# Kernel optimization log

Measured on AMD Instinct MI355X. Metric: run time of the kernel, lower is better.

## Reference

```python
import jax, jax.numpy as jnp
import numpy as np

B, N, E, Q = 4, 10000, 160000, 256
D, M, U, H, P = 128, 64, 126, 128, 7  # node_dim, msg_sz, update_sz, mlp hidden, pose dim
MSG_STEPS = 3
NUM_COPIES = 1


def setup_inputs() -> dict:
    key = jax.random.key(0)
    ks = jax.random.split(key, 12)
    return {
        "nodes_states": jax.random.normal(ks[0], (B, N, D), jnp.float32),
        "query_poses": jax.random.normal(ks[1], (B, Q, P), jnp.float32),
        "attn": jax.random.uniform(ks[2], (B, Q, N), jnp.float32) / N,
        "edge_sources": jax.random.randint(ks[3], (E,), 0, N),
        "edge_sinks": jax.random.randint(ks[4], (E,), 0, N),
        "w1e": jax.random.normal(ks[5], (2 * D, H), jnp.float32) * 0.05,
        "b1e": jnp.zeros((H,), jnp.float32),
        "w2e": jax.random.normal(ks[6], (H, M), jnp.float32) * 0.05,
        "b2e": jnp.zeros((M,), jnp.float32),
        "w1n": jax.random.normal(ks[7], (D + M, H), jnp.float32) * 0.05,
        "b1n": jnp.zeros((H,), jnp.float32),
        "w2n": jax.random.normal(ks[8], (H, U), jnp.float32) * 0.05,
        "b2n": jnp.zeros((U,), jnp.float32),
    }


def reference(nodes_states, query_poses, attn, edge_sources, edge_sinks,
              w1e, b1e, w2e, b2e, w1n, b1n, w2n, b2n):
    def step(states, _):
        # gather endpoint states: [B, E, 2*D]
        einp = jnp.concatenate([states[:, edge_sources], states[:, edge_sinks]], axis=-1)
        # edge MLP -> per-edge messages [B, E, M]
        msg = jax.nn.relu(einp @ w1e + b1e) @ w2e + b2e
        # scatter-add messages to sink nodes [B, N, M]
        incoming = jnp.zeros((states.shape[0], N, M), states.dtype).at[:, edge_sinks].add(msg)
        # node MLP update [B, N, U]
        ninp = jnp.concatenate([incoming, states], axis=-1)
        upd = jax.nn.relu(ninp @ w1n + b1n) @ w2n + b2n
        # only the last U channels (state part, not positions) are updated
        states = states.at[:, :, -U:].add(upd)
        return states, None

    states, _ = jax.lax.scan(step, nodes_states, None, length=MSG_STEPS)
    extraction = jnp.einsum('bqn,bnd->bqd', attn, states)  # interpolation readout
    return jnp.concatenate([query_poses] * NUM_COPIES + [extraction], axis=-1)
```

## Files before the change

kernel.cpp:

```cpp
#include <hip/hip_runtime.h>

#define Bx 4
#define Nn 10000
#define Ee 160000
#define Qq 256
#define Dd 128
#define Mm 64
#define Uu 126
#define Hh 128
#define Pp 7

#define KG 1252

typedef unsigned short u16;
typedef __bf16 bf16x8 __attribute__((ext_vector_type(8)));
typedef float f32x4 __attribute__((ext_vector_type(4)));

__device__ __forceinline__ float b2f(u16 h){
  unsigned u = ((unsigned)h) << 16; float f; __builtin_memcpy(&f, &u, 4); return f;
}
__device__ __forceinline__ u16 f2b(float f){
  __bf16 h = (__bf16)f; u16 r; __builtin_memcpy(&r, &h, 2); return r;
}
__device__ __forceinline__ float ldin(const void* p, long i, int flag){
  return flag ? b2f(((const u16*)p)[i]) : ((const float*)p)[i];
}

__global__ void probe_kernel(const void* in0, int* flag){
  if (threadIdx.x == 0 && blockIdx.x == 0){
    const u16* p = (const u16*)in0;
    int cnt = 0;
    for (int i = 0; i < 256; i++){
      float a = fabsf(b2f(p[i]));
      if (a > 0.0009765625f && a < 32.0f) cnt++;
    }
    *flag = (cnt >= 240) ? 1 : 0;
  }
}

__global__ void prep_kernel(const void* w1e, const void* b1e, const void* w2e, const void* b2e,
                            const void* w1n, const void* b1n, const void* w2n, const void* b2n,
                            const int* __restrict__ flag,
                            u16* w1e_s, u16* w2e_s, u16* w1n_s, u16* w2n_s,
                            float* b1e_f, float* b2e_f, float* b1n_f, float* b2n_f)
{
  int f = *flag;
  for (int idx = blockIdx.x * blockDim.x + threadIdx.x; idx < 82368; idx += gridDim.x * blockDim.x){
    if (idx < 32768){
      int k = idx >> 7, h = idx & 127;
      w1e_s[(k >> 3) * 1024 + h * 8 + (k & 7)] = f2b(ldin(w1e, idx, f));
    } else if (idx < 40960){
      int i2 = idx - 32768; int k = i2 >> 6, m2 = i2 & 63;
      w2e_s[(k >> 3) * 512 + m2 * 8 + (k & 7)] = f2b(ldin(w2e, i2, f));
    } else if (idx < 65536){
      int i2 = idx - 40960; int k = i2 >> 7, h = i2 & 127;
      w1n_s[(k >> 3) * 1024 + h * 8 + (k & 7)] = f2b(ldin(w1n, i2, f));
    } else if (idx < 81920){
      int i2 = idx - 65536; int k = i2 >> 7, u = i2 & 127;
      float v = (u < 126) ? ldin(w2n, (long)k * 126 + u, f) : 0.f;
      w2n_s[(k >> 3) * 1024 + u * 8 + (k & 7)] = f2b(v);
    } else if (idx < 82048){ b1e_f[idx - 81920] = ldin(b1e, idx - 81920, f); }
    else if (idx < 82112){ b2e_f[idx - 82048] = ldin(b2e, idx - 82048, f); }
    else if (idx < 82240){ b1n_f[idx - 82112] = ldin(b1n, idx - 82112, f); }
    else { int j = idx - 82240; b2n_f[j] = (j < 126) ? ldin(b2n, j, f) : 0.f; }
  }
}

__global__ void init_states_kernel(const void* in0, const int* __restrict__ flag,
                                   const int* __restrict__ snk,
                                   float* __restrict__ sf, u16* __restrict__ sbm,
                                   int* __restrict__ cnt)
{
  int f = *flag;
  const long total = (long)Bx * Nn * Dd;
  long base = (long)blockIdx.x * blockDim.x + threadIdx.x;
  for (long i = base; i < total; i += (long)gridDim.x * blockDim.x){
    float v = ldin(in0, i, f);
    sf[i] = v; sbm[i] = f2b(v);
  }
  for (long i = base; i < Ee; i += (long)gridDim.x * blockDim.x)
    atomicAdd(&cnt[snk[(int)i]], 1);
}

__global__ void scan_kernel(const int* __restrict__ cnt, int* __restrict__ rowp){
  __shared__ int tot[1024];
  int t = threadIdx.x;
  int base = t * 10;
  int local[10]; int s = 0;
  #pragma unroll
  for (int i = 0; i < 10; i++){
    int v = (base + i < Nn) ? cnt[base + i] : 0;
    local[i] = s; s += v;
  }
  tot[t] = s;
  __syncthreads();
  for (int o = 1; o < 1024; o <<= 1){
    int v = (t >= o) ? tot[t - o] : 0;
    __syncthreads();
    tot[t] += v;
    __syncthreads();
  }
  int prefix = (t == 0) ? 0 : tot[t - 1];
  #pragma unroll
  for (int i = 0; i < 10; i++)
    if (base + i < Nn) rowp[base + i] = prefix + local[i];
  if (t == 1023) rowp[Nn] = tot[1023];
}
__global__ void fill_kernel(const int* __restrict__ src, const int* __restrict__ snk,
                            const int* __restrict__ rowp, int* __restrict__ cnt,
                            int* __restrict__ psrc){
  int i = blockIdx.x * blockDim.x + threadIdx.x;
  if (i < Ee){
    int s = snk[i];
    int p = rowp[s] + atomicAdd(&cnt[s], 1);
    psrc[p] = src[i];
  }
}

__global__ __launch_bounds__(256) void xform_kernel(
  const u16* __restrict__ sbm, const u16* __restrict__ w1s,
  const float* __restrict__ b1f, u16* __restrict__ xab)
{
  __shared__ __align__(16) u16 w1h[16384];
  __shared__ __align__(16) u16 Yt[64 * 136];
  int tid = threadIdx.x;
  int b = (blockIdx.x & 7) >> 1;
  int nt = ((blockIdx.x >> 3) << 1) + (blockIdx.x & 1);
  if (nt >= 157) return;
  int n0 = nt * 64;
  int w = tid >> 6, lane = tid & 63, m = lane & 15, quad = lane >> 4;
  int n = n0 + w * 16 + m;
  int nld = n < Nn ? n : Nn - 1;
  const u16* srow = sbm + (((size_t)b * Nn + nld) << 7);

  bf16x8 a[4];
  #pragma unroll
  for (int lk = 0; lk < 4; lk++) a[lk] = *(const bf16x8*)(srow + lk * 32 + quad * 8);

  const f32x4 z4 = {0.f, 0.f, 0.f, 0.f};
  int row_l = lane >> 2, seg = lane & 3;
  int nst = n0 + w * 16 + row_l;

  #pragma unroll
  for (int half = 0; half < 2; half++){
    __syncthreads();
    {
      const uint4* g = (const uint4*)(w1s + half * 16384);
      uint4* l = (uint4*)w1h;
      #pragma unroll
      for (int i = 0; i < 8; i++) l[tid + i * 256] = g[tid + i * 256];
    }
    __syncthreads();
    f32x4 acc[8];
    #pragma unroll
    for (int ct = 0; ct < 8; ct++) acc[ct] = z4;
    #pragma unroll
    for (int lk = 0; lk < 4; lk++){
      #pragma unroll
      for (int ct = 0; ct < 8; ct++){
        bf16x8 bv = *(const bf16x8*)(w1h + (((lk * 4 + quad) << 7) + ct * 16 + m) * 8);
        acc[ct] = __builtin_amdgcn_mfma_f32_16x16x32_bf16(a[lk], bv, acc[ct], 0, 0, 0);
      }
    }
    #pragma unroll
    for (int ct = 0; ct < 8; ct++){
      float bb = (half == 0) ? b1f[ct * 16 + m] : 0.f;
      #pragma unroll
      for (int i = 0; i < 4; i++)
        Yt[(w * 16 + quad * 4 + i) * 136 + ct * 16 + m] = f2b(acc[ct][i] + bb);
    }
    if (nst < Nn){
      const uint4* tp = (const uint4*)(Yt + (w * 16 + row_l) * 136 + seg * 32);
      uint4 x0 = tp[0], x1 = tp[1], x2 = tp[2], x3 = tp[3];
      uint4* gp = (uint4*)(xab + ((size_t)b * Nn + nst) * 256 + half * 128 + seg * 32);
      gp[0] = x0; gp[1] = x1; gp[2] = x2; gp[3] = x3;
    }
  }
}

__global__ __launch_bounds__(256) void node_kernel(
  float* __restrict__ sf, u16* __restrict__ sbm, const u16* __restrict__ xab,
  const int* __restrict__ rowp, const int* __restrict__ psrc,
  const u16* __restrict__ w2es, const float* __restrict__ b2ef,
  const u16* __restrict__ w1s, const u16* __restrict__ w2s,
  const float* __restrict__ b1f, const float* __restrict__ b2f2)
{
  __shared__ __align__(16) u16 ninp[64 * 200];
  __shared__ __align__(16) u16 hsYt[64 * 136];
  int b = (blockIdx.x & 7) >> 1;
  int nt = ((blockIdx.x >> 3) << 1) + (blockIdx.x & 1);
  if (nt >= 157) return;
  int n0 = nt * 64;
  int tid = threadIdx.x;

  {
    int nl = tid >> 2, part = tid & 3;
    int n = n0 + nl;
    float acc[32];
    #pragma unroll
    for (int i = 0; i < 32; i++) acc[i] = 0.f;
    if (n < Nn){
      float xbf[32];
      {
        const uint4* xp = (const uint4*)(xab + ((size_t)b * Nn + n) * 256 + 128 + part * 32);
        union { uint4 v; u16 h[8]; } q[4];
        q[0].v = xp[0]; q[1].v = xp[1]; q[2].v = xp[2]; q[3].v = xp[3];
        #pragma unroll
        for (int t4 = 0; t4 < 4; t4++)
          #pragma unroll
          for (int j = 0; j < 8; j++) xbf[t4 * 8 + j] = b2f(q[t4].h[j]);
      }
      int r0 = rowp[n], r1 = rowp[n + 1];
      const u16* xb0 = xab + (size_t)b * Nn * 256;
      for (int r = r0; r < r1; r++){
        int s = psrc[r];
        const uint4* xp = (const uint4*)(xb0 + (size_t)s * 256 + part * 32);
        union { uint4 v; u16 h[8]; } q[4];
        q[0].v = xp[0]; q[1].v = xp[1]; q[2].v = xp[2]; q[3].v = xp[3];
        #pragma unroll
        for (int t4 = 0; t4 < 4; t4++)
          #pragma unroll
          for (int j = 0; j < 8; j++){
            float v = b2f(q[t4].h[j]) + xbf[t4 * 8 + j];
            acc[t4 * 8 + j] += v > 0.f ? v : 0.f;
          }
      }
    }
    union { u16 h[32]; uint4 v[4]; } hb;
    #pragma unroll
    for (int i = 0; i < 32; i++) hb.h[i] = f2b(acc[i]);
    uint4* hp = (uint4*)(hsYt + nl * 136 + part * 32);
    hp[0] = hb.v[0]; hp[1] = hb.v[1]; hp[2] = hb.v[2]; hp[3] = hb.v[3];
    uint4* dp = (uint4*)(ninp + nl * 200 + 64 + part * 32);
    if (n < Nn){
      const uint4* sp = (const uint4*)(sbm + (((size_t)b * Nn + n) << 7) + part * 32);
      #pragma unroll
      for (int i = 0; i < 4; i++) dp[i] = sp[i];
    } else {
      uint4 zz = {0, 0, 0, 0};
      #pragma unroll
      for (int i = 0; i < 4; i++) dp[i] = zz;
    }
  }

  int w = tid >> 6, lane = tid & 63, m = lane & 15, quad = lane >> 4;
  const f32x4 z4 = {0.f, 0.f, 0.f, 0.f};

  {
    f32x4 acc[4];
    #pragma unroll
    for (int ct = 0; ct < 4; ct++) acc[ct] = z4;
    #pragma unroll
    for (int ks = 0; ks < 4; ks++){
      bf16x8 a = *(const bf16x8*)(hsYt + (w * 16 + m) * 136 + ks * 32 + quad * 8);
      #pragma unroll
      for (int ct = 0; ct < 4; ct++){
        bf16x8 bv = *(const bf16x8*)(w2es + (((ks * 4 + quad) << 6) + ct * 16 + m) * 8);
        acc[ct] = __builtin_amdgcn_mfma_f32_16x16x32_bf16(a, bv, acc[ct], 0, 0, 0);
      }
    }
    #pragma unroll
    for (int i = 0; i < 4; i++){
      int n = n0 + w * 16 + quad * 4 + i;
      float deg = (n < Nn) ? (float)(rowp[n + 1] - rowp[n]) : 0.f;
      #pragma unroll
      for (int ct = 0; ct < 4; ct++)
        ninp[(w * 16 + quad * 4 + i) * 200 + ct * 16 + m] = f2b(acc[ct][i] + deg * b2ef[ct * 16 + m]);
    }
  }

  f32x4 acc1[8];
  #pragma unroll
  for (int ct = 0; ct < 8; ct++) acc1[ct] = z4;
  #pragma unroll 1
  for (int ks = 0; ks < 6; ks++){
    bf16x8 a = *(const bf16x8*)(ninp + (w * 16 + m) * 200 + ks * 32 + quad * 8);
    #pragma unroll
    for (int ct = 0; ct < 8; ct++){
      bf16x8 bv = *(const bf16x8*)(w1s + (((ks * 4 + quad) << 7) + ct * 16 + m) * 8);
      acc1[ct] = __builtin_amdgcn_mfma_f32_16x16x32_bf16(a, bv, acc1[ct], 0, 0, 0);
    }
  }
  #pragma unroll
  for (int ct = 0; ct < 8; ct++){
    float bb = b1f[ct * 16 + m];
    #pragma unroll
    for (int i = 0; i < 4; i++){
      float v = acc1[ct][i] + bb;
      v = v > 0.f ? v : 0.f;
      hsYt[(w * 16 + quad * 4 + i) * 136 + ct * 16 + m] = f2b(v);
    }
  }
  f32x4 acc2[8];
  #pragma unroll
  for (int ct = 0; ct < 8; ct++) acc2[ct] = z4;
  #pragma unroll 1
  for (int ko = 0; ko < 4; ko++){
    bf16x8 a2 = *(const bf16x8*)(hsYt + (w * 16 + m) * 136 + ko * 32 + quad * 8);
    #pragma unroll
    for (int ct = 0; ct < 8; ct++){
      bf16x8 bv = *(const bf16x8*)(w2s + (((ko * 4 + quad) << 7) + ct * 16 + m) * 8);
      acc2[ct] = __builtin_amdgcn_mfma_f32_16x16x32_bf16(a2, bv, acc2[ct], 0, 0, 0);
    }
  }
  #pragma unroll
  for (int ct = 0; ct < 8; ct++){
    int u = ct * 16 + m;
    if (u < 126){
      float bb = b2f2[u];
      #pragma unroll
      for (int i = 0; i < 4; i++){
        int n = n0 + w * 16 + quad * 4 + i;
        if (n < Nn){
          size_t idx = (((size_t)b * Nn + n) << 7) + 2 + u;
          float v = sf[idx] + acc2[ct][i] + bb;
          sf[idx] = v;
          sbm[idx] = f2b(v);
        }
      }
    }
  }
}

__global__ void swz_s_kernel(const u16* __restrict__ sbm, u16* __restrict__ sswz)
{
  const long total = (long)Bx * KG * 128;
  for (long i = (long)blockIdx.x * blockDim.x + threadIdx.x; i < total; i += (long)gridDim.x * blockDim.x){
    int d = (int)(i & 127); long r = i >> 7;
    int kg = (int)(r % KG); int b = (int)(r / KG);
    union { u16 h[8]; uint4 v[2]; } t;
    if (kg < 1250){
      #pragma unroll
      for (int j = 0; j < 8; j++)
        t.h[j] = sbm[(((size_t)b * Nn + kg * 8 + j) << 7) + d];
    } else {
      #pragma unroll
      for (int j = 0; j < 8; j++) t.h[j] = 0;
    }
    *(uint4*)(sswz + i * 8) = t.v[0];
    *(uint4*)(sswz + i * 8 + 8) = t.v[1];
  }
}
__global__ __launch_bounds__(256) void extract2_kernel(
  const void* __restrict__ attn, const int* __restrict__ flag,
  const u16* __restrict__ sswz, float* __restrict__ part)
{
  int f = *flag;
  int blk = blockIdx.x;
  int kc = blk & 31, qt = (blk >> 5) & 3, b = blk >> 7;
  int tid = threadIdx.x, w = tid >> 6, lane = tid & 63, m = lane & 15, quad = lane >> 4;
  int qr = qt * 4 + w, q0 = qr * 16;
  int kg0 = kc * 40;
  int nsteps = (kc == 31) ? 3 : 10;
  long arow = ((long)(b * Qq + q0 + m)) * Nn;
  const u16* ab16 = (const u16*)attn + arow;
  const float* af32 = (const float*)attn + arow;
  const u16* sbase = sswz + ((size_t)b) * KG * 1024;
  f32x4 acc[8];
  const f32x4 z4 = {0.f, 0.f, 0.f, 0.f};
  #pragma unroll
  for (int ct = 0; ct < 8; ct++) acc[ct] = z4;
  #pragma unroll 1
  for (int t = 0; t < nsteps; t++){
    int kg = kg0 + t * 4 + quad;
    int kgc = kg < KG ? kg : 0;
    bf16x8 a;
    if (kg < 1250){
      if (f){
        a = *(const bf16x8*)(ab16 + kg * 8);
      } else {
        const float* ap = af32 + kg * 8;
        float4 p0 = *(const float4*)ap;
        float4 p1 = *(const float4*)(ap + 4);
        a[0] = (__bf16)p0.x; a[1] = (__bf16)p0.y; a[2] = (__bf16)p0.z; a[3] = (__bf16)p0.w;
        a[4] = (__bf16)p1.x; a[5] = (__bf16)p1.y; a[6] = (__bf16)p1.z; a[7] = (__bf16)p1.w;
      }
    } else {
      #pragma unroll
      for (int j = 0; j < 8; j++) a[j] = (__bf16)0.f;
    }
    #pragma unroll
    for (int ct = 0; ct < 8; ct++){
      bf16x8 bv = *(const bf16x8*)(sbase + ((size_t)kgc * 128 + ct * 16 + m) * 8);
      acc[ct] = __builtin_amdgcn_mfma_f32_16x16x32_bf16(a, bv, acc[ct], 0, 0, 0);
    }
  }
  #pragma unroll
  for (int ct = 0; ct < 8; ct++){
    #pragma unroll
    for (int i = 0; i < 4; i++)
      part[(((size_t)(kc * 4 + b)) * Qq + q0 + quad * 4 + i) * 128 + ct * 16 + m] = acc[ct][i];
  }
}

__global__ void final_kernel(const void* __restrict__ poses, const int* __restrict__ flag,
                             const float* __restrict__ part, void* __restrict__ out)
{
  int f = *flag;
  const long total = (long)Bx * Qq * (Pp + Dd);
  for (long idx = (long)blockIdx.x * blockDim.x + threadIdx.x; idx < total; idx += (long)gridDim.x * blockDim.x){
    int j = (int)(idx % (Pp + Dd));
    long bq = idx / (Pp + Dd);
    float v;
    if (j < Pp){
      v = ldin(poses, bq * Pp + j, f);
    } else {
      int dd = j - Pp;
      int b = (int)(bq >> 8), q = (int)(bq & 255);
      v = 0.f;
      #pragma unroll
      for (int kc = 0; kc < 32; kc++)
        v += part[(((size_t)(kc * 4 + b) * Qq + q) << 7) + dd];
    }
    if (f) ((u16*)out)[idx] = f2b(v);
    else ((float*)out)[idx] = v;
  }
}

extern "C" void kernel_launch(void* const* d_in, const int* in_sizes, int n_in,
                              void* d_out, int out_size, void* d_ws, size_t ws_size,
                              hipStream_t stream)
{
  const void* in_states = d_in[0];
  const void* in_poses  = d_in[1];
  const void* in_attn   = d_in[2];
  const int*  in_src    = (const int*)d_in[3];
  const int*  in_snk    = (const int*)d_in[4];
  const void* in_w1e = d_in[5];  const void* in_b1e = d_in[6];
  const void* in_w2e = d_in[7];  const void* in_b2e = d_in[8];
  const void* in_w1n = d_in[9];  const void* in_b1n = d_in[10];
  const void* in_w2n = d_in[11]; const void* in_b2n = d_in[12];

  char* ws = (char*)d_ws;
  size_t off = 0;
  auto alloc = [&](size_t bytes){ size_t o = off; off = (off + bytes + 255) & ~(size_t)255; return o; };
  size_t o_sf   = alloc((size_t)Bx * Nn * Dd * 4);
  size_t o_sb   = alloc((size_t)Bx * Nn * Dd * 2);
  size_t o_xab  = alloc((size_t)Bx * Nn * 256 * 2);
  size_t o_rowp = alloc((size_t)(Nn + 1) * 4);
  size_t o_rcnt = alloc((size_t)Nn * 4);
  size_t o_psrc = alloc((size_t)Ee * 4);
  size_t o_w1e  = alloc(32768 * 2);
  size_t o_w2e  = alloc(8192 * 2);
  size_t o_w1n  = alloc(24576 * 2);
  size_t o_w2n  = alloc(16384 * 2);
  size_t o_b1e  = alloc(128 * 4);
  size_t o_b2e  = alloc(64 * 4);
  size_t o_b1n  = alloc(128 * 4);
  size_t o_b2n  = alloc(128 * 4);
  size_t o_flag = alloc(4);

  size_t sswzB = (size_t)Bx * KG * 128 * 8 * 2;
  size_t partB = (size_t)32 * Bx * Qq * Dd * 4;
  size_t o_sswz = alloc(sswzB);
  size_t o_part = alloc(partB);

  float* sf    = (float*)(ws + o_sf);
  u16*   sbm   = (u16*)(ws + o_sb);
  u16*   xab   = (u16*)(ws + o_xab);
  int*   rowp  = (int*)(ws + o_rowp);
  int*   rcnt  = (int*)(ws + o_rcnt);
  int*   psrc  = (int*)(ws + o_psrc);
  u16*   w1e_s = (u16*)(ws + o_w1e);
  u16*   w2e_s = (u16*)(ws + o_w2e);
  u16*   w1n_s = (u16*)(ws + o_w1n);
  u16*   w2n_s = (u16*)(ws + o_w2n);
  float* b1e_f = (float*)(ws + o_b1e);
  float* b2e_f = (float*)(ws + o_b2e);
  float* b1n_f = (float*)(ws + o_b1n);
  float* b2n_f = (float*)(ws + o_b2n);
  int*   flag  = (int*)(ws + o_flag);
  u16*   sswz  = (u16*)(ws + o_sswz);
  float* part  = (float*)(ws + o_part);

  hipMemsetAsync(rcnt, 0, (size_t)Nn * 4, stream);
  probe_kernel<<<1, 64, 0, stream>>>(in_states, flag);
  prep_kernel<<<322, 256, 0, stream>>>(in_w1e, in_b1e, in_w2e, in_b2e,
                                       in_w1n, in_b1n, in_w2n, in_b2n, flag,
                                       w1e_s, w2e_s, w1n_s, w2n_s,
                                       b1e_f, b2e_f, b1n_f, b2n_f);
  init_states_kernel<<<1024, 256, 0, stream>>>(in_states, flag, in_snk, sf, sbm, rcnt);

  scan_kernel<<<1, 1024, 0, stream>>>(rcnt, rowp);
  hipMemsetAsync(rcnt, 0, (size_t)Nn * 4, stream);
  fill_kernel<<<(Ee + 255) / 256, 256, 0, stream>>>(in_src, in_snk, rowp, rcnt, psrc);

  for (int step = 0; step < 3; step++){
    xform_kernel<<<632, 256, 0, stream>>>(sbm, w1e_s, b1e_f, xab);
    node_kernel<<<632, 256, 0, stream>>>(sf, sbm, xab, rowp, psrc,
                                         w2e_s, b2e_f,
                                         w1n_s, w2n_s, b1n_f, b2n_f);
  }
  swz_s_kernel<<<2504, 256, 0, stream>>>(sbm, sswz);
  extract2_kernel<<<512, 256, 0, stream>>>(in_attn, flag, sswz, part);
  final_kernel<<<540, 256, 0, stream>>>(in_poses, flag, part, d_out);
}
```

Before: 375.8 us.

## Split edge-transform buffer, halve node tile, and unroll neighbor gather by four

The interleaved xab buffer becomes two separate arrays, xa (source half) and xb (sink half), so the per-edge gather reads a compact 256-byte row stride. The node kernel now handles 32 nodes per block with 8 threads per node, launches twice as many blocks, and unrolls the CSR neighbor loop four-wide with masked duplicate loads so more gathers are in flight. The xb-half writes and the final sf/sbm updates use nontemporal stores and loads. In exchange, half of each block's threads sit idle during the MFMA phase, and a 4-edge unroll wastes loads on short neighbor lists.

Result: slower. 445.4 us (+18.5%).

```diff
diff --git a/kernel.cpp b/kernel.cpp
--- a/kernel.cpp
+++ b/kernel.cpp
@@ -15,6 +15,7 @@
 typedef unsigned short u16;
 typedef __bf16 bf16x8 __attribute__((ext_vector_type(8)));
 typedef float f32x4 __attribute__((ext_vector_type(4)));
+typedef unsigned int u32x4 __attribute__((ext_vector_type(4)));
 
 __device__ __forceinline__ float b2f(u16 h){
   unsigned u = ((unsigned)h) << 16; float f; __builtin_memcpy(&f, &u, 4); return f;
@@ -119,7 +120,7 @@
 
 __global__ __launch_bounds__(256) void xform_kernel(
   const u16* __restrict__ sbm, const u16* __restrict__ w1s,
-  const float* __restrict__ b1f, u16* __restrict__ xab)
+  const float* __restrict__ b1f, u16* __restrict__ xa, u16* __restrict__ xb)
 {
   __shared__ __align__(16) u16 w1h[16384];
   __shared__ __align__(16) u16 Yt[64 * 136];
@@ -170,78 +171,118 @@
         Yt[(w * 16 + quad * 4 + i) * 136 + ct * 16 + m] = f2b(acc[ct][i] + bb);
     }
     if (nst < Nn){
-      const uint4* tp = (const uint4*)(Yt + (w * 16 + row_l) * 136 + seg * 32);
-      uint4 x0 = tp[0], x1 = tp[1], x2 = tp[2], x3 = tp[3];
-      uint4* gp = (uint4*)(xab + ((size_t)b * Nn + nst) * 256 + half * 128 + seg * 32);
-      gp[0] = x0; gp[1] = x1; gp[2] = x2; gp[3] = x3;
+      const u16* tb = Yt + (w * 16 + row_l) * 136 + seg * 8;
+      u32x4 x0 = *(const u32x4*)(tb);
+      u32x4 x1 = *(const u32x4*)(tb + 32);
+      u32x4 x2 = *(const u32x4*)(tb + 64);
+      u32x4 x3 = *(const u32x4*)(tb + 96);
+      u16* gb = (half == 0 ? xa : xb) + ((size_t)b * Nn + nst) * 128 + seg * 8;
+      if (half == 0){
+        *(u32x4*)(gb)      = x0;
+        *(u32x4*)(gb + 32) = x1;
+        *(u32x4*)(gb + 64) = x2;
+        *(u32x4*)(gb + 96) = x3;
+      } else {
+        __builtin_nontemporal_store(x0, (u32x4*)(gb));
+        __builtin_nontemporal_store(x1, (u32x4*)(gb + 32));
+        __builtin_nontemporal_store(x2, (u32x4*)(gb + 64));
+        __builtin_nontemporal_store(x3, (u32x4*)(gb + 96));
+      }
     }
   }
 }
 
 __global__ __launch_bounds__(256) void node_kernel(
-  float* __restrict__ sf, u16* __restrict__ sbm, const u16* __restrict__ xab,
+  float* __restrict__ sf, u16* __restrict__ sbm,
+  const u16* __restrict__ xa, const u16* __restrict__ xb,
   const int* __restrict__ rowp, const int* __restrict__ psrc,
   const u16* __restrict__ w2es, const float* __restrict__ b2ef,
   const u16* __restrict__ w1s, const u16* __restrict__ w2s,
   const float* __restrict__ b1f, const float* __restrict__ b2f2)
 {
-  __shared__ __align__(16) u16 ninp[64 * 200];
-  __shared__ __align__(16) u16 hsYt[64 * 136];
+  __shared__ __align__(16) u16 ninp[32 * 200];
+  __shared__ __align__(16) u16 hsYt[32 * 136];
   int b = (blockIdx.x & 7) >> 1;
   int nt = ((blockIdx.x >> 3) << 1) + (blockIdx.x & 1);
-  if (nt >= 157) return;
-  int n0 = nt * 64;
+  int n0 = nt * 32;
+  if (n0 >= Nn + 31) return;
   int tid = threadIdx.x;
 
   {
-    int nl = tid >> 2, part = tid & 3;
+    int nl = tid >> 3, part = tid & 7;
     int n = n0 + nl;
-    float acc[32];
-    #pragma unroll
-    for (int i = 0; i < 32; i++) acc[i] = 0.f;
+    float acc[16];
+    #pragma unroll
+    for (int i = 0; i < 16; i++) acc[i] = 0.f;
     if (n < Nn){
-      float xbf[32];
+      float xbf[16];
       {
-        const uint4* xp = (const uint4*)(xab + ((size_t)b * Nn + n) * 256 + 128 + part * 32);
-        union { uint4 v; u16 h[8]; } q[4];
-        q[0].v = xp[0]; q[1].v = xp[1]; q[2].v = xp[2]; q[3].v = xp[3];
+        const u16* xp = xb + ((size_t)b * Nn + n) * 128 + part * 8;
+        union { uint4 v; u16 h[8]; } q0, q1;
+        q0.v = *(const uint4*)(xp);
+        q1.v = *(const uint4*)(xp + 64);
         #pragma unroll
-        for (int t4 = 0; t4 < 4; t4++)
-          #pragma unroll
-          for (int j = 0; j < 8; j++) xbf[t4 * 8 + j] = b2f(q[t4].h[j]);
-      }
-      int r0 = rowp[n], r1 = rowp[n + 1];
-      const u16* xb0 = xab + (size_t)b * Nn * 256;
-      for (int r = r0; r < r1; r++){
-        int s = psrc[r];
-        const uint4* xp = (const uint4*)(xb0 + (size_t)s * 256 + part * 32);
-        union { uint4 v; u16 h[8]; } q[4];
-        q[0].v = xp[0]; q[1].v = xp[1]; q[2].v = xp[2]; q[3].v = xp[3];
+        for (int j = 0; j < 8; j++){ xbf[j] = b2f(q0.h[j]); xbf[8 + j] = b2f(q1.h[j]); }
+      }
+      int r0v = rowp[n], r1v = rowp[n + 1];
+      const u16* xaB = xa + (size_t)b * Nn * 128 + part * 8;
+      for (int r = r0v; r < r1v; r += 4){
+        int rb = r + 1 < r1v ? r + 1 : r0v;
+        int rc = r + 2 < r1v ? r + 2 : r0v;
+        int rd = r + 3 < r1v ? r + 3 : r0v;
+        float wb = r + 1 < r1v ? 1.f : 0.f;
+        float wc = r + 2 < r1v ? 1.f : 0.f;
+        float wd = r + 3 < r1v ? 1.f : 0.f;
+        int sa = psrc[r], sb2 = psrc[rb], sc = psrc[rc], sd = psrc[rd];
+        const u16* pa = xaB + (size_t)sa * 128;
+        const u16* pb = xaB + (size_t)sb2 * 128;
+        const u16* pc = xaB + (size_t)sc * 128;
+        const u16* pd = xaB + (size_t)sd * 128;
+        union { uint4 v; u16 h[8]; } qa0, qa1, qb0, qb1, qc0, qc1, qd0, qd1;
+        qa0.v = *(const uint4*)(pa); qa1.v = *(const uint4*)(pa + 64);
+        qb0.v = *(const uint4*)(pb); qb1.v = *(const uint4*)(pb + 64);
+        qc0.v = *(const uint4*)(pc); qc1.v = *(const uint4*)(pc + 64);
+        qd0.v = *(const uint4*)(pd); qd1.v = *(const uint4*)(pd + 64);
         #pragma unroll
-        for (int t4 = 0; t4 < 4; t4++)
-          #pragma unroll
-          for (int j = 0; j < 8; j++){
-            float v = b2f(q[t4].h[j]) + xbf[t4 * 8 + j];
-            acc[t4 * 8 + j] += v > 0.f ? v : 0.f;
-          }
-      }
-    }
-    union { u16 h[32]; uint4 v[4]; } hb;
-    #pragma unroll
-    for (int i = 0; i < 32; i++) hb.h[i] = f2b(acc[i]);
-    uint4* hp = (uint4*)(hsYt + nl * 136 + part * 32);
-    hp[0] = hb.v[0]; hp[1] = hb.v[1]; hp[2] = hb.v[2]; hp[3] = hb.v[3];
-    uint4* dp = (uint4*)(ninp + nl * 200 + 64 + part * 32);
+        for (int j = 0; j < 8; j++){
+          float va0 = b2f(qa0.h[j]) + xbf[j];
+          float va1 = b2f(qa1.h[j]) + xbf[8 + j];
+          acc[j]     += va0 > 0.f ? va0 : 0.f;
+          acc[8 + j] += va1 > 0.f ? va1 : 0.f;
+          float vb0 = b2f(qb0.h[j]) + xbf[j];
+          float vb1 = b2f(qb1.h[j]) + xbf[8 + j];
+          acc[j]     = fmaf(wb, vb0 > 0.f ? vb0 : 0.f, acc[j]);
+          acc[8 + j] = fmaf(wb, vb1 > 0.f ? vb1 : 0.f, acc[8 + j]);
+          float vc0 = b2f(qc0.h[j]) + xbf[j];
+          float vc1 = b2f(qc1.h[j]) + xbf[8 + j];
+          acc[j]     = fmaf(wc, vc0 > 0.f ? vc0 : 0.f, acc[j]);
+          acc[8 + j] = fmaf(wc, vc1 > 0.f ? vc1 : 0.f, acc[8 + j]);
+          float vd0 = b2f(qd0.h[j]) + xbf[j];
+          float vd1 = b2f(qd1.h[j]) + xbf[8 + j];
+          acc[j]     = fmaf(wd, vd0 > 0.f ? vd0 : 0.f, acc[j]);
+          acc[8 + j] = fmaf(wd, vd1 > 0.f ? vd1 : 0.f, acc[8 + j]);
+        }
+      }
+    }
+    union { u16 h[16]; uint4 v[2]; } hb;
+    #pragma unroll
+    for (int i = 0; i < 16; i++) hb.h[i] = f2b(acc[i]);
+    u16* hp = hsYt + nl * 136 + part * 8;
+    *(uint4*)(hp)      = hb.v[0];
+    *(uint4*)(hp + 64) = hb.v[1];
+    u16* dp = ninp + nl * 200 + 64 + part * 8;
     if (n < Nn){
-      const uint4* sp = (const uint4*)(sbm + (((size_t)b * Nn + n) << 7) + part * 32);
-      #pragma unroll
-      for (int i = 0; i < 4; i++) dp[i] = sp[i];
+      const u16* sp = sbm + (((size_t)b * Nn + n) << 7) + part * 8;
+      *(uint4*)(dp)      = *(const uint4*)(sp);
+      *(uint4*)(dp + 64) = *(const uint4*)(sp + 64);
     } else {
       uint4 zz = {0, 0, 0, 0};
-      #pragma unroll
-      for (int i = 0; i < 4; i++) dp[i] = zz;
-    }
-  }
+      *(uint4*)(dp)      = zz;
+      *(uint4*)(dp + 64) = zz;
+    }
+  }
+  __syncthreads();
+  if (tid >= 128) return;
 
   int w = tid >> 6, lane = tid & 63, m = lane & 15, quad = lane >> 4;
   const f32x4 z4 = {0.f, 0.f, 0.f, 0.f};
@@ -313,9 +354,9 @@
         int n = n0 + w * 16 + quad * 4 + i;
         if (n < Nn){
           size_t idx = (((size_t)b * Nn + n) << 7) + 2 + u;
-          float v = sf[idx] + acc2[ct][i] + bb;
-          sf[idx] = v;
-          sbm[idx] = f2b(v);
+          float v = __builtin_nontemporal_load(&sf[idx]) + acc2[ct][i] + bb;
+          __builtin_nontemporal_store(v, &sf[idx]);
+          __builtin_nontemporal_store(f2b(v), &sbm[idx]);
         }
       }
     }
@@ -436,7 +477,8 @@
   auto alloc = [&](size_t bytes){ size_t o = off; off = (off + bytes + 255) & ~(size_t)255; return o; };
   size_t o_sf   = alloc((size_t)Bx * Nn * Dd * 4);
   size_t o_sb   = alloc((size_t)Bx * Nn * Dd * 2);
-  size_t o_xab  = alloc((size_t)Bx * Nn * 256 * 2);
+  size_t o_xa   = alloc((size_t)Bx * Nn * 128 * 2);
+  size_t o_xb   = alloc((size_t)Bx * Nn * 128 * 2);
   size_t o_rowp = alloc((size_t)(Nn + 1) * 4);
   size_t o_rcnt = alloc((size_t)Nn * 4);
   size_t o_psrc = alloc((size_t)Ee * 4);
@@ -457,7 +499,8 @@
 
   float* sf    = (float*)(ws + o_sf);
   u16*   sbm   = (u16*)(ws + o_sb);
-  u16*   xab   = (u16*)(ws + o_xab);
+  u16*   xa    = (u16*)(ws + o_xa);
+  u16*   xb    = (u16*)(ws + o_xb);
   int*   rowp  = (int*)(ws + o_rowp);
   int*   rcnt  = (int*)(ws + o_rcnt);
   int*   psrc  = (int*)(ws + o_psrc);
@@ -486,10 +529,10 @@
   fill_kernel<<<(Ee + 255) / 256, 256, 0, stream>>>(in_src, in_snk, rowp, rcnt, psrc);
 
   for (int step = 0; step < 3; step++){
-    xform_kernel<<<632, 256, 0, stream>>>(sbm, w1e_s, b1e_f, xab);
-    node_kernel<<<632, 256, 0, stream>>>(sf, sbm, xab, rowp, psrc,
-                                         w2e_s, b2e_f,
-                                         w1n_s, w2n_s, b1n_f, b2n_f);
+    xform_kernel<<<632, 256, 0, stream>>>(sbm, w1e_s, b1e_f, xa, xb);
+    node_kernel<<<1256, 256, 0, stream>>>(sf, sbm, xa, xb, rowp, psrc,
+                                          w2e_s, b2e_f,
+                                          w1n_s, w2n_s, b1n_f, b2n_f);
   }
   swz_s_kernel<<<2504, 256, 0, stream>>>(sbm, sswz);
   extract2_kernel<<<512, 256, 0, stream>>>(in_attn, flag, sswz, part);
```

## Store gathered edge pre-activations in FP8 and halve node tile size

Applied to the files above, without the earlier changes.

The per-source half of the first edge-MLP layer (gathered once per edge) is now written as FP8 with a permuted column order, and the w2e swizzle is changed to match. The sink half stays bf16 in a separate buffer. The intent is to halve the bytes of the irregular per-edge gather, which dominates node_kernel. The node kernel also processes 32 nodes per block with 8 threads per node, over twice as many blocks, and only half its threads run the MLP stage. The tradeoff is lower precision on the edge pre-activations, plus idle threads in the MFMA phase.

New measurement: 370.3 us. Within noise of the previous version (-1.5%).

```diff
diff --git a/kernel.cpp b/kernel.cpp
--- a/kernel.cpp
+++ b/kernel.cpp
@@ -15,6 +15,7 @@
 typedef unsigned short u16;
 typedef __bf16 bf16x8 __attribute__((ext_vector_type(8)));
 typedef float f32x4 __attribute__((ext_vector_type(4)));
+typedef float f32x2 __attribute__((ext_vector_type(2)));
 
 __device__ __forceinline__ float b2f(u16 h){
   unsigned u = ((unsigned)h) << 16; float f; __builtin_memcpy(&f, &u, 4); return f;
@@ -51,7 +52,7 @@
       w1e_s[(k >> 3) * 1024 + h * 8 + (k & 7)] = f2b(ldin(w1e, idx, f));
     } else if (idx < 40960){
       int i2 = idx - 32768; int k = i2 >> 6, m2 = i2 & 63;
-      w2e_s[(k >> 3) * 512 + m2 * 8 + (k & 7)] = f2b(ldin(w2e, i2, f));
+      w2e_s[(k & 15) * 512 + m2 * 8 + (k >> 4)] = f2b(ldin(w2e, i2, f));
     } else if (idx < 65536){
       int i2 = idx - 40960; int k = i2 >> 7, h = i2 & 127;
       w1n_s[(k >> 3) * 1024 + h * 8 + (k & 7)] = f2b(ldin(w1n, i2, f));
@@ -119,10 +120,9 @@
 
 __global__ __launch_bounds__(256) void xform_kernel(
   const u16* __restrict__ sbm, const u16* __restrict__ w1s,
-  const float* __restrict__ b1f, u16* __restrict__ xab)
+  const float* __restrict__ b1f, unsigned char* __restrict__ xa, u16* __restrict__ xb)
 {
   __shared__ __align__(16) u16 w1h[16384];
-  __shared__ __align__(16) u16 Yt[64 * 136];
   int tid = threadIdx.x;
   int b = (blockIdx.x & 7) >> 1;
   int nt = ((blockIdx.x >> 3) << 1) + (blockIdx.x & 1);
@@ -138,8 +138,10 @@
   for (int lk = 0; lk < 4; lk++) a[lk] = *(const bf16x8*)(srow + lk * 32 + quad * 8);
 
   const f32x4 z4 = {0.f, 0.f, 0.f, 0.f};
-  int row_l = lane >> 2, seg = lane & 3;
-  int nst = n0 + w * 16 + row_l;
+  int rbase = n0 + w * 16 + quad * 4;
+  float bb[8];
+  #pragma unroll
+  for (int ct = 0; ct < 8; ct++) bb[ct] = b1f[ct * 16 + m];
 
   #pragma unroll
   for (int half = 0; half < 2; half++){
@@ -162,86 +164,104 @@
         acc[ct] = __builtin_amdgcn_mfma_f32_16x16x32_bf16(a[lk], bv, acc[ct], 0, 0, 0);
       }
     }
-    #pragma unroll
-    for (int ct = 0; ct < 8; ct++){
-      float bb = (half == 0) ? b1f[ct * 16 + m] : 0.f;
-      #pragma unroll
-      for (int i = 0; i < 4; i++)
-        Yt[(w * 16 + quad * 4 + i) * 136 + ct * 16 + m] = f2b(acc[ct][i] + bb);
-    }
-    if (nst < Nn){
-      const uint4* tp = (const uint4*)(Yt + (w * 16 + row_l) * 136 + seg * 32);
-      uint4 x0 = tp[0], x1 = tp[1], x2 = tp[2], x3 = tp[3];
-      uint4* gp = (uint4*)(xab + ((size_t)b * Nn + nst) * 256 + half * 128 + seg * 32);
-      gp[0] = x0; gp[1] = x1; gp[2] = x2; gp[3] = x3;
+    if (half == 0){
+      #pragma unroll
+      for (int i = 0; i < 4; i++){
+        int r = rbase + i;
+        if (r < Nn){
+          int d0 = __builtin_amdgcn_cvt_pk_fp8_f32(acc[0][i] + bb[0], acc[1][i] + bb[1], 0, false);
+          d0 = __builtin_amdgcn_cvt_pk_fp8_f32(acc[2][i] + bb[2], acc[3][i] + bb[3], d0, true);
+          int d1 = __builtin_amdgcn_cvt_pk_fp8_f32(acc[4][i] + bb[4], acc[5][i] + bb[5], 0, false);
+          d1 = __builtin_amdgcn_cvt_pk_fp8_f32(acc[6][i] + bb[6], acc[7][i] + bb[7], d1, true);
+          uint2 v; v.x = (unsigned)d0; v.y = (unsigned)d1;
+          *(uint2*)(xa + ((size_t)b * Nn + r) * 128 + m * 8) = v;
+        }
+      }
+    } else {
+      #pragma unroll
+      for (int i = 0; i < 4; i++){
+        int r = rbase + i;
+        if (r < Nn){
+          union { u16 h[8]; uint4 v; } t;
+          #pragma unroll
+          for (int ct = 0; ct < 8; ct++) t.h[ct] = f2b(acc[ct][i]);
+          *(uint4*)(xb + ((size_t)b * Nn + r) * 128 + m * 8) = t.v;
+        }
+      }
     }
   }
 }
 
 __global__ __launch_bounds__(256) void node_kernel(
-  float* __restrict__ sf, u16* __restrict__ sbm, const u16* __restrict__ xab,
+  float* __restrict__ sf, u16* __restrict__ sbm,
+  const unsigned char* __restrict__ xa, const u16* __restrict__ xb,
   const int* __restrict__ rowp, const int* __restrict__ psrc,
   const u16* __restrict__ w2es, const float* __restrict__ b2ef,
   const u16* __restrict__ w1s, const u16* __restrict__ w2s,
   const float* __restrict__ b1f, const float* __restrict__ b2f2)
 {
-  __shared__ __align__(16) u16 ninp[64 * 200];
-  __shared__ __align__(16) u16 hsYt[64 * 136];
+  __shared__ __align__(16) u16 ninp[32 * 200];
+  __shared__ __align__(16) u16 hsYt[32 * 136];
   int b = (blockIdx.x & 7) >> 1;
   int nt = ((blockIdx.x >> 3) << 1) + (blockIdx.x & 1);
-  if (nt >= 157) return;
-  int n0 = nt * 64;
+  int n0 = nt * 32;
+  if (n0 >= Nn + 31) return;
   int tid = threadIdx.x;
 
   {
-    int nl = tid >> 2, part = tid & 3;
+    int nl = tid >> 3, part = tid & 7;
     int n = n0 + nl;
-    float acc[32];
-    #pragma unroll
-    for (int i = 0; i < 32; i++) acc[i] = 0.f;
+    float acc[16];
+    #pragma unroll
+    for (int i = 0; i < 16; i++) acc[i] = 0.f;
     if (n < Nn){
-      float xbf[32];
+      float xbf[16];
       {
-        const uint4* xp = (const uint4*)(xab + ((size_t)b * Nn + n) * 256 + 128 + part * 32);
-        union { uint4 v; u16 h[8]; } q[4];
-        q[0].v = xp[0]; q[1].v = xp[1]; q[2].v = xp[2]; q[3].v = xp[3];
+        const u16* xp = xb + ((size_t)b * Nn + n) * 128 + part * 16;
+        union { uint4 v; u16 h[8]; } q0, q1;
+        q0.v = *(const uint4*)(xp);
+        q1.v = *(const uint4*)(xp + 8);
         #pragma unroll
-        for (int t4 = 0; t4 < 4; t4++)
-          #pragma unroll
-          for (int j = 0; j < 8; j++) xbf[t4 * 8 + j] = b2f(q[t4].h[j]);
-      }
-      int r0 = rowp[n], r1 = rowp[n + 1];
-      const u16* xb0 = xab + (size_t)b * Nn * 256;
-      for (int r = r0; r < r1; r++){
+        for (int j = 0; j < 8; j++){ xbf[j] = b2f(q0.h[j]); xbf[8 + j] = b2f(q1.h[j]); }
+      }
+      int r0v = rowp[n], r1v = rowp[n + 1];
+      const unsigned char* xaB = xa + (size_t)b * Nn * 128 + part * 16;
+      for (int r = r0v; r < r1v; r++){
         int s = psrc[r];
-        const uint4* xp = (const uint4*)(xb0 + (size_t)s * 256 + part * 32);
-        union { uint4 v; u16 h[8]; } q[4];
-        q[0].v = xp[0]; q[1].v = xp[1]; q[2].v = xp[2]; q[3].v = xp[3];
-        #pragma unroll
-        for (int t4 = 0; t4 < 4; t4++)
-          #pragma unroll
-          for (int j = 0; j < 8; j++){
-            float v = b2f(q[t4].h[j]) + xbf[t4 * 8 + j];
-            acc[t4 * 8 + j] += v > 0.f ? v : 0.f;
-          }
-      }
-    }
-    union { u16 h[32]; uint4 v[4]; } hb;
-    #pragma unroll
-    for (int i = 0; i < 32; i++) hb.h[i] = f2b(acc[i]);
-    uint4* hp = (uint4*)(hsYt + nl * 136 + part * 32);
-    hp[0] = hb.v[0]; hp[1] = hb.v[1]; hp[2] = hb.v[2]; hp[3] = hb.v[3];
-    uint4* dp = (uint4*)(ninp + nl * 200 + 64 + part * 32);
+        uint4 q = *(const uint4*)(xaB + (size_t)s * 128);
+        #define ACC4(W, B) { \
+          f32x2 lo = __builtin_amdgcn_cvt_pk_f32_fp8((int)(W), false); \
+          f32x2 hi = __builtin_amdgcn_cvt_pk_f32_fp8((int)(W), true);  \
+          float v0 = lo[0] + xbf[B + 0]; acc[B + 0] += fmaxf(v0, 0.f); \
+          float v1 = lo[1] + xbf[B + 1]; acc[B + 1] += fmaxf(v1, 0.f); \
+          float v2 = hi[0] + xbf[B + 2]; acc[B + 2] += fmaxf(v2, 0.f); \
+          float v3 = hi[1] + xbf[B + 3]; acc[B + 3] += fmaxf(v3, 0.f); }
+        ACC4(q.x, 0)
+        ACC4(q.y, 4)
+        ACC4(q.z, 8)
+        ACC4(q.w, 12)
+        #undef ACC4
+      }
+    }
+    union { u16 h[16]; uint4 v[2]; } hb;
+    #pragma unroll
+    for (int i = 0; i < 16; i++) hb.h[i] = f2b(acc[i]);
+    u16* hp = hsYt + nl * 136 + part * 16;
+    *(uint4*)(hp)     = hb.v[0];
+    *(uint4*)(hp + 8) = hb.v[1];
+    u16* dp = ninp + nl * 200 + 64 + part * 16;
     if (n < Nn){
-      const uint4* sp = (const uint4*)(sbm + (((size_t)b * Nn + n) << 7) + part * 32);
-      #pragma unroll
-      for (int i = 0; i < 4; i++) dp[i] = sp[i];
+      const u16* sp = sbm + (((size_t)b * Nn + n) << 7) + part * 16;
+      *(uint4*)(dp)     = *(const uint4*)(sp);
+      *(uint4*)(dp + 8) = *(const uint4*)(sp + 8);
     } else {
       uint4 zz = {0, 0, 0, 0};
-      #pragma unroll
-      for (int i = 0; i < 4; i++) dp[i] = zz;
-    }
-  }
+      *(uint4*)(dp)     = zz;
+      *(uint4*)(dp + 8) = zz;
+    }
+  }
+  __syncthreads();
+  if (tid >= 128) return;
 
   int w = tid >> 6, lane = tid & 63, m = lane & 15, quad = lane >> 4;
   const f32x4 z4 = {0.f, 0.f, 0.f, 0.f};
@@ -436,7 +456,8 @@
   auto alloc = [&](size_t bytes){ size_t o = off; off = (off + bytes + 255) & ~(size_t)255; return o; };
   size_t o_sf   = alloc((size_t)Bx * Nn * Dd * 4);
   size_t o_sb   = alloc((size_t)Bx * Nn * Dd * 2);
-  size_t o_xab  = alloc((size_t)Bx * Nn * 256 * 2);
+  size_t o_xa   = alloc((size_t)Bx * Nn * 128);
+  size_t o_xb   = alloc((size_t)Bx * Nn * 128 * 2);
   size_t o_rowp = alloc((size_t)(Nn + 1) * 4);
   size_t o_rcnt = alloc((size_t)Nn * 4);
   size_t o_psrc = alloc((size_t)Ee * 4);
@@ -457,7 +478,8 @@
 
   float* sf    = (float*)(ws + o_sf);
   u16*   sbm   = (u16*)(ws + o_sb);
-  u16*   xab   = (u16*)(ws + o_xab);
+  unsigned char* xa = (unsigned char*)(ws + o_xa);
+  u16*   xb    = (u16*)(ws + o_xb);
   int*   rowp  = (int*)(ws + o_rowp);
   int*   rcnt  = (int*)(ws + o_rcnt);
   int*   psrc  = (int*)(ws + o_psrc);
@@ -486,10 +508,10 @@
   fill_kernel<<<(Ee + 255) / 256, 256, 0, stream>>>(in_src, in_snk, rowp, rcnt, psrc);
 
   for (int step = 0; step < 3; step++){
-    xform_kernel<<<632, 256, 0, stream>>>(sbm, w1e_s, b1e_f, xab);
-    node_kernel<<<632, 256, 0, stream>>>(sf, sbm, xab, rowp, psrc,
-                                         w2e_s, b2e_f,
-                                         w1n_s, w2n_s, b1n_f, b2n_f);
+    xform_kernel<<<632, 256, 0, stream>>>(sbm, w1e_s, b1e_f, xa, xb);
+    node_kernel<<<1256, 256, 0, stream>>>(sf, sbm, xa, xb, rowp, psrc,
+                                          w2e_s, b2e_f,
+                                          w1n_s, w2n_s, b1n_f, b2n_f);
   }
   swz_s_kernel<<<2504, 256, 0, stream>>>(sbm, sswz);
   extract2_kernel<<<512, 256, 0, stream>>>(in_attn, flag, sswz, part);
```

## Process all batches per node tile so edge gather reuses CSR traversal

Applied to the files above, without the earlier changes.

Splits the transformed edge-input buffer into separate source and sink planes, and reorganises node_kernel so each block handles 16 nodes across all 4 batches instead of 64 nodes of one batch. Each CSR edge list (rowp/psrc) is traversed once and gathers all four batch rows per source, with 16 lanes per node covering the 128 channels. This amortises index loads and improves gather coalescing. The cost is more register pressure from four accumulator sets and a different block-to-row mapping in the MFMA stages, where the wave index now selects the batch.

New measurement: 379.3 us. No clear change (+0.9%).

```diff
diff --git a/kernel.cpp b/kernel.cpp
--- a/kernel.cpp
+++ b/kernel.cpp
@@ -119,7 +119,7 @@
 
 __global__ __launch_bounds__(256) void xform_kernel(
   const u16* __restrict__ sbm, const u16* __restrict__ w1s,
-  const float* __restrict__ b1f, u16* __restrict__ xab)
+  const float* __restrict__ b1f, u16* __restrict__ xa, u16* __restrict__ xb)
 {
   __shared__ __align__(16) u16 w1h[16384];
   __shared__ __align__(16) u16 Yt[64 * 136];
@@ -170,16 +170,23 @@
         Yt[(w * 16 + quad * 4 + i) * 136 + ct * 16 + m] = f2b(acc[ct][i] + bb);
     }
     if (nst < Nn){
-      const uint4* tp = (const uint4*)(Yt + (w * 16 + row_l) * 136 + seg * 32);
-      uint4 x0 = tp[0], x1 = tp[1], x2 = tp[2], x3 = tp[3];
-      uint4* gp = (uint4*)(xab + ((size_t)b * Nn + nst) * 256 + half * 128 + seg * 32);
-      gp[0] = x0; gp[1] = x1; gp[2] = x2; gp[3] = x3;
+      const u16* tb = Yt + (w * 16 + row_l) * 136 + seg * 8;
+      uint4 x0 = *(const uint4*)(tb);
+      uint4 x1 = *(const uint4*)(tb + 32);
+      uint4 x2 = *(const uint4*)(tb + 64);
+      uint4 x3 = *(const uint4*)(tb + 96);
+      u16* gb = (half == 0 ? xa : xb) + ((size_t)b * Nn + nst) * 128 + seg * 8;
+      *(uint4*)(gb)      = x0;
+      *(uint4*)(gb + 32) = x1;
+      *(uint4*)(gb + 64) = x2;
+      *(uint4*)(gb + 96) = x3;
     }
   }
 }
 
 __global__ __launch_bounds__(256) void node_kernel(
-  float* __restrict__ sf, u16* __restrict__ sbm, const u16* __restrict__ xab,
+  float* __restrict__ sf, u16* __restrict__ sbm,
+  const u16* __restrict__ xa, const u16* __restrict__ xb,
   const int* __restrict__ rowp, const int* __restrict__ psrc,
   const u16* __restrict__ w2es, const float* __restrict__ b2ef,
   const u16* __restrict__ w1s, const u16* __restrict__ w2s,
@@ -187,61 +194,70 @@
 {
   __shared__ __align__(16) u16 ninp[64 * 200];
   __shared__ __align__(16) u16 hsYt[64 * 136];
-  int b = (blockIdx.x & 7) >> 1;
-  int nt = ((blockIdx.x >> 3) << 1) + (blockIdx.x & 1);
-  if (nt >= 157) return;
-  int n0 = nt * 64;
+  const size_t PSu = (size_t)Nn * 128;
+  int n0 = blockIdx.x * 16;
   int tid = threadIdx.x;
 
   {
-    int nl = tid >> 2, part = tid & 3;
+    int nl = tid >> 4, part = tid & 15;
     int n = n0 + nl;
-    float acc[32];
-    #pragma unroll
-    for (int i = 0; i < 32; i++) acc[i] = 0.f;
-    if (n < Nn){
-      float xbf[32];
-      {
-        const uint4* xp = (const uint4*)(xab + ((size_t)b * Nn + n) * 256 + 128 + part * 32);
-        union { uint4 v; u16 h[8]; } q[4];
-        q[0].v = xp[0]; q[1].v = xp[1]; q[2].v = xp[2]; q[3].v = xp[3];
-        #pragma unroll
-        for (int t4 = 0; t4 < 4; t4++)
-          #pragma unroll
-          for (int j = 0; j < 8; j++) xbf[t4 * 8 + j] = b2f(q[t4].h[j]);
+    float acc0[8], acc1[8], acc2[8], acc3[8];
+    #pragma unroll
+    for (int i = 0; i < 8; i++){ acc0[i] = 0.f; acc1[i] = 0.f; acc2[i] = 0.f; acc3[i] = 0.f; }
+    float xbf0[8], xbf1[8], xbf2[8], xbf3[8];
+    {
+      const u16* xp = xb + (size_t)n * 128 + part * 8;
+      union { uint4 v; u16 h[8]; } q0, q1, q2, q3;
+      q0.v = *(const uint4*)(xp);
+      q1.v = *(const uint4*)(xp + PSu);
+      q2.v = *(const uint4*)(xp + 2 * PSu);
+      q3.v = *(const uint4*)(xp + 3 * PSu);
+      #pragma unroll
+      for (int j = 0; j < 8; j++){
+        xbf0[j] = b2f(q0.h[j]); xbf1[j] = b2f(q1.h[j]);
+        xbf2[j] = b2f(q2.h[j]); xbf3[j] = b2f(q3.h[j]);
       }
-      int r0 = rowp[n], r1 = rowp[n + 1];
-      const u16* xb0 = xab + (size_t)b * Nn * 256;
-      for (int r = r0; r < r1; r++){
-        int s = psrc[r];
-        const uint4* xp = (const uint4*)(xb0 + (size_t)s * 256 + part * 32);
-        union { uint4 v; u16 h[8]; } q[4];
-        q[0].v = xp[0]; q[1].v = xp[1]; q[2].v = xp[2]; q[3].v = xp[3];
-        #pragma unroll
-        for (int t4 = 0; t4 < 4; t4++)
-          #pragma unroll
-          for (int j = 0; j < 8; j++){
-            float v = b2f(q[t4].h[j]) + xbf[t4 * 8 + j];
-            acc[t4 * 8 + j] += v > 0.f ? v : 0.f;
-          }
+    }
+    int r0v = rowp[n], r1v = rowp[n + 1];
+    const u16* xap = xa + part * 8;
+    for (int r = r0v; r < r1v; r++){
+      int s = psrc[r];
+      const u16* p0 = xap + (size_t)s * 128;
+      union { uint4 v; u16 h[8]; } qa, qb, qc, qd;
+      qa.v = *(const uint4*)(p0);
+      qb.v = *(const uint4*)(p0 + PSu);
+      qc.v = *(const uint4*)(p0 + 2 * PSu);
+      qd.v = *(const uint4*)(p0 + 3 * PSu);
+      #pragma unroll
+      for (int j = 0; j < 8; j++){
+        float v0 = b2f(qa.h[j]) + xbf0[j]; acc0[j] += fmaxf(v0, 0.f);
+        float v1 = b2f(qb.h[j]) + xbf1[j]; acc1[j] += fmaxf(v1, 0.f);
+        float v2 = b2f(qc.h[j]) + xbf2[j]; acc2[j] += fmaxf(v2, 0.f);
+        float v3 = b2f(qd.h[j]) + xbf3[j]; acc3[j] += fmaxf(v3, 0.f);
       }
     }
-    union { u16 h[32]; uint4 v[4]; } hb;
-    #pragma unroll
-    for (int i = 0; i < 32; i++) hb.h[i] = f2b(acc[i]);
-    uint4* hp = (uint4*)(hsYt + nl * 136 + part * 32);
-    hp[0] = hb.v[0]; hp[1] = hb.v[1]; hp[2] = hb.v[2]; hp[3] = hb.v[3];
-    uint4* dp = (uint4*)(ninp + nl * 200 + 64 + part * 32);
-    if (n < Nn){
-      const uint4* sp = (const uint4*)(sbm + (((size_t)b * Nn + n) << 7) + part * 32);
-      #pragma unroll
-      for (int i = 0; i < 4; i++) dp[i] = sp[i];
-    } else {
-      uint4 zz = {0, 0, 0, 0};
-      #pragma unroll
-      for (int i = 0; i < 4; i++) dp[i] = zz;
-    }
-  }
+    {
+      union { u16 h[8]; uint4 v; } hb;
+      #pragma unroll
+      for (int i = 0; i < 8; i++) hb.h[i] = f2b(acc0[i]);
+      *(uint4*)(hsYt + (0 * 16 + nl) * 136 + part * 8) = hb.v;
+      #pragma unroll
+      for (int i = 0; i < 8; i++) hb.h[i] = f2b(acc1[i]);
+      *(uint4*)(hsYt + (1 * 16 + nl) * 136 + part * 8) = hb.v;
+      #pragma unroll
+      for (int i = 0; i < 8; i++) hb.h[i] = f2b(acc2[i]);
+      *(uint4*)(hsYt + (2 * 16 + nl) * 136 + part * 8) = hb.v;
+      #pragma unroll
+      for (int i = 0; i < 8; i++) hb.h[i] = f2b(acc3[i]);
+      *(uint4*)(hsYt + (3 * 16 + nl) * 136 + part * 8) = hb.v;
+    }
+    #pragma unroll
+    for (int bb = 0; bb < 4; bb++){
+      const u16* sp = sbm + (((size_t)bb * Nn + n) << 7) + part * 8;
+      *(uint4*)(ninp + (bb * 16 + nl) * 200 + 64 + part * 8) = *(const uint4*)(sp);
+    }
+  }
+  __syncthreads();
 
   int w = tid >> 6, lane = tid & 63, m = lane & 15, quad = lane >> 4;
   const f32x4 z4 = {0.f, 0.f, 0.f, 0.f};
@@ -261,8 +277,8 @@
     }
     #pragma unroll
     for (int i = 0; i < 4; i++){
-      int n = n0 + w * 16 + quad * 4 + i;
-      float deg = (n < Nn) ? (float)(rowp[n + 1] - rowp[n]) : 0.f;
+      int n = n0 + quad * 4 + i;
+      float deg = (float)(rowp[n + 1] - rowp[n]);
       #pragma unroll
       for (int ct = 0; ct < 4; ct++)
         ninp[(w * 16 + quad * 4 + i) * 200 + ct * 16 + m] = f2b(acc[ct][i] + deg * b2ef[ct * 16 + m]);
@@ -310,13 +326,11 @@
       float bb = b2f2[u];
       #pragma unroll
       for (int i = 0; i < 4; i++){
-        int n = n0 + w * 16 + quad * 4 + i;
-        if (n < Nn){
-          size_t idx = (((size_t)b * Nn + n) << 7) + 2 + u;
-          float v = sf[idx] + acc2[ct][i] + bb;
-          sf[idx] = v;
-          sbm[idx] = f2b(v);
-        }
+        int n = n0 + quad * 4 + i;
+        size_t idx = (((size_t)w * Nn + n) << 7) + 2 + u;
+        float v = sf[idx] + acc2[ct][i] + bb;
+        sf[idx] = v;
+        sbm[idx] = f2b(v);
       }
     }
   }
@@ -436,7 +450,8 @@
   auto alloc = [&](size_t bytes){ size_t o = off; off = (off + bytes + 255) & ~(size_t)255; return o; };
   size_t o_sf   = alloc((size_t)Bx * Nn * Dd * 4);
   size_t o_sb   = alloc((size_t)Bx * Nn * Dd * 2);
-  size_t o_xab  = alloc((size_t)Bx * Nn * 256 * 2);
+  size_t o_xa   = alloc((size_t)Bx * Nn * 128 * 2);
+  size_t o_xb   = alloc((size_t)Bx * Nn * 128 * 2);
   size_t o_rowp = alloc((size_t)(Nn + 1) * 4);
   size_t o_rcnt = alloc((size_t)Nn * 4);
   size_t o_psrc = alloc((size_t)Ee * 4);
@@ -457,7 +472,8 @@
 
   float* sf    = (float*)(ws + o_sf);
   u16*   sbm   = (u16*)(ws + o_sb);
-  u16*   xab   = (u16*)(ws + o_xab);
+  u16*   xa    = (u16*)(ws + o_xa);
+  u16*   xb    = (u16*)(ws + o_xb);
   int*   rowp  = (int*)(ws + o_rowp);
   int*   rcnt  = (int*)(ws + o_rcnt);
   int*   psrc  = (int*)(ws + o_psrc);
@@ -486,8 +502,8 @@
   fill_kernel<<<(Ee + 255) / 256, 256, 0, stream>>>(in_src, in_snk, rowp, rcnt, psrc);
 
   for (int step = 0; step < 3; step++){
-    xform_kernel<<<632, 256, 0, stream>>>(sbm, w1e_s, b1e_f, xab);
-    node_kernel<<<632, 256, 0, stream>>>(sf, sbm, xab, rowp, psrc,
+    xform_kernel<<<632, 256, 0, stream>>>(sbm, w1e_s, b1e_f, xa, xb);
+    node_kernel<<<625, 256, 0, stream>>>(sf, sbm, xa, xb, rowp, psrc,
                                          w2e_s, b2e_f,
                                          w1n_s, w2n_s, b1n_f, b2n_f);
   }
```
